# Optimization experiments

Hardware: AMD Instinct MI355X
Metric: run time of the kernel (lower is better)

## Reference

```python
import jax, jax.numpy as jnp
import numpy as np

B, SQ, SK, D, H, DFF, L = 8, 1024, 1024, 512, 8, 2048, 2
HD = D // H  # head dim = 64
EPS = 1e-5


def _ln(x, g, b):
    mu = jnp.mean(x, axis=-1, keepdims=True)
    var = jnp.mean((x - mu) ** 2, axis=-1, keepdims=True)
    return (x - mu) * jax.lax.rsqrt(var + EPS) * g + b


def setup_inputs() -> dict:
    key = jax.random.key(0)
    ks = jax.random.split(key, 16)
    std = 0.02
    inp = {
        'q': jax.random.normal(ks[0], (B, SQ, D), jnp.float32),
        'k': jax.random.normal(ks[1], (B, SK, D), jnp.float32),
        'v': jax.random.normal(ks[2], (B, SK, D), jnp.float32),
        # per-layer stacked params (weights stored [in, out])
        'WQ': jax.random.normal(ks[3], (L, D, D), jnp.float32) * std,
        'bQ': jnp.zeros((L, D), jnp.float32),
        'WK': jax.random.normal(ks[4], (L, D, D), jnp.float32) * std,
        'bK': jnp.zeros((L, D), jnp.float32),
        'WV': jax.random.normal(ks[5], (L, D, D), jnp.float32) * std,
        'bV': jnp.zeros((L, D), jnp.float32),
        'WO': jax.random.normal(ks[6], (L, D, D), jnp.float32) * std,
        'bO': jnp.zeros((L, D), jnp.float32),
        'Wf1': jax.random.normal(ks[7], (L, D, DFF), jnp.float32) * std,
        'bf1': jnp.zeros((L, DFF), jnp.float32),
        'Wf2': jax.random.normal(ks[8], (L, DFF, D), jnp.float32) * std,
        'bf2': jnp.zeros((L, D), jnp.float32),
        'ln1_g': jnp.ones((L, D), jnp.float32),
        'ln1_b': jnp.zeros((L, D), jnp.float32),
        'ln2_g': jnp.ones((L, D), jnp.float32),
        'ln2_b': jnp.zeros((L, D), jnp.float32),
        'scale': jnp.full((L,), HD ** -0.5, jnp.float32),       # self.scale init
        'extra_scale': jnp.ones((L,), jnp.float32),             # self.extra_scale init
        'gate_attn': jnp.ones((L,), jnp.float32),
        'gate_ffn': jnp.ones((L,), jnp.float32),
    }
    return inp


def reference(q, k, v, WQ, bQ, WK, bK, WV, bV, WO, bO, Wf1, bf1, Wf2, bf2,
              ln1_g, ln1_b, ln2_g, ln2_b, scale, extra_scale, gate_attn, gate_ffn):
    prev = None  # Realformer residual attention scores
    for i in range(L):
        # QKV projections -> [B, H, S, HD]
        qh = (jnp.einsum('bsd,de->bse', q, WQ[i]) + bQ[i]).reshape(B, SQ, H, HD).transpose(0, 2, 1, 3)
        kh = (jnp.einsum('bsd,de->bse', k, WK[i]) + bK[i]).reshape(B, SK, H, HD).transpose(0, 2, 1, 3)
        vh = (jnp.einsum('bsd,de->bse', v, WV[i]) + bV[i]).reshape(B, SK, H, HD).transpose(0, 2, 1, 3)
        eff_scale = scale[i] * jnp.clip(extra_scale[i], 0.01, 50.0)
        scores = jnp.einsum('bhqd,bhkd->bhqk', qh, kh) * eff_scale  # [B,H,SQ,SK]
        if prev is not None:
            scores = scores + prev
        attn = jax.nn.softmax(scores, axis=-1)
        out = jnp.einsum('bhqk,bhkd->bhqd', attn, vh)
        out = out.transpose(0, 2, 1, 3).reshape(B, SQ, D)
        out = jnp.einsum('bsd,de->bse', out, WO[i]) + bO[i]
        # gated residual + post-norm
        q = q + jax.nn.softplus(gate_attn[i]) * out
        q = _ln(q, ln1_g[i], ln1_b[i])
        # FFN (exact gelu like torch default)
        ff = jax.nn.gelu(jnp.einsum('bsd,df->bsf', q, Wf1[i]) + bf1[i], approximate=False)
        ff = jnp.einsum('bsf,fd->bsd', ff, Wf2[i]) + bf2[i]
        q = q + jax.nn.softplus(gate_ffn[i]) * ff
        q = _ln(q, ln2_g[i], ln2_b[i])
        prev = scores
    return q
```

## Files before the change

kernel.cpp:

```cpp
#include <hip/hip_runtime.h>

#define B_   8
#define SQ_  1024
#define SK_  1024
#define D_   512
#define H_   8
#define DFF_ 2048
#define L_   2
#define HD_  64
#define M_   8192

typedef __bf16 bf16;
using bf16x8 = __attribute__((ext_vector_type(8))) __bf16;
using f32x4  = __attribute__((ext_vector_type(4))) float;

__device__ inline f32x4 mfma16(bf16x8 a, bf16x8 b, f32x4 c) {
  return __builtin_amdgcn_mfma_f32_16x16x32_bf16(a, b, c, 0, 0, 0);
}

__device__ __forceinline__ void gl2lds16(const bf16* g, bf16* l) {
  __builtin_amdgcn_global_load_lds(
      (const __attribute__((address_space(1))) void*)g,
      (__attribute__((address_space(3))) void*)l, 16, 0, 0);
}

__device__ __forceinline__ float gelu_fast(float x) {
  float u = 1.5957691216f * (x + 0.044715f * x * x * x);
  return x / (1.0f + __expf(-u));
}

struct TP4 { const float* in[4]; bf16* out[4]; };
__global__ __launch_bounds__(256) void transpose4_k(TP4 p) {
  __shared__ bf16 tile[32][33];
  int z = blockIdx.z, wsel = z >> 1, l = z & 1;
  const float* inp  = p.in[wsel]  + (size_t)l * D_ * D_;
  bf16*        outp = p.out[wsel] + (size_t)l * D_ * D_;
  int c0 = blockIdx.x * 32, r0 = blockIdx.y * 32;
  int tx = threadIdx.x & 31, ty = threadIdx.x >> 5;
#pragma unroll
  for (int i = 0; i < 32; i += 8)
    tile[ty + i][tx] = (bf16)inp[(size_t)(r0 + ty + i) * D_ + c0 + tx];
  __syncthreads();
#pragma unroll
  for (int i = 0; i < 32; i += 8)
    outp[(size_t)(c0 + ty + i) * D_ + r0 + tx] = tile[tx][ty + i];
}

__global__ __launch_bounds__(256) void transpose_k(
    const float* __restrict__ in, bf16* __restrict__ out, int R, int C) {
  __shared__ bf16 tile[32][33];
  const float* inp  = in  + (size_t)blockIdx.z * R * C;
  bf16*        outp = out + (size_t)blockIdx.z * R * C;
  int c0 = blockIdx.x * 32, r0 = blockIdx.y * 32;
  int tx = threadIdx.x & 31, ty = threadIdx.x >> 5;
#pragma unroll
  for (int i = 0; i < 32; i += 8)
    tile[ty + i][tx] = (bf16)inp[(size_t)(r0 + ty + i) * C + c0 + tx];
  __syncthreads();
#pragma unroll
  for (int i = 0; i < 32; i += 8)
    outp[(size_t)(c0 + ty + i) * R + r0 + tx] = tile[tx][ty + i];
}

__global__ __launch_bounds__(256) void f2b3_k(
    const float* __restrict__ a, const float* __restrict__ b,
    const float* __restrict__ c, bf16* __restrict__ oa,
    bf16* __restrict__ ob, bf16* __restrict__ oc) {
  int which = blockIdx.y;
  const float* in = (which == 0) ? a : (which == 1) ? b : c;
  bf16* out = (which == 0) ? oa : (which == 1) ? ob : oc;
  int i = (blockIdx.x * 256 + threadIdx.x) * 4;
  float4 v = *(const float4*)&in[i];
  out[i] = (bf16)v.x; out[i + 1] = (bf16)v.y;
  out[i + 2] = (bf16)v.z; out[i + 3] = (bf16)v.w;
}

struct G256 { const bf16* A; const bf16* Bt; const float* bias; bf16* C; };

#define MFB(mh) \
  _Pragma("unroll") \
  for (int mi = 0; mi < 4; mi++) { \
    _Pragma("unroll") \
    for (int ni = 0; ni < 4; ni++) \
      acc[(mh) * 4 + mi][ni] = mfma16(a[mi], b[ni], acc[(mh) * 4 + mi][ni]); \
  }

#define PHASE(s, mh, STAGE, VM) \
  { \
    if ((mh) == 0) { \
      a[0] = ldA(s, 0); a[1] = ldA(s, 1); a[2] = ldA(s, 2); a[3] = ldA(s, 3); \
      b[0] = ldB(s, 0); b[1] = ldB(s, 1); b[2] = ldB(s, 2); b[3] = ldB(s, 3); \
    } else { \
      a[0] = ldA(s, 4); a[1] = ldA(s, 5); a[2] = ldA(s, 6); a[3] = ldA(s, 7); \
    } \
    STAGE; \
    VM; \
    __builtin_amdgcn_s_barrier(); \
    asm volatile("s_waitcnt lgkmcnt(0)" ::: "memory"); \
    __builtin_amdgcn_sched_barrier(0); \
    __builtin_amdgcn_s_setprio(1); \
    MFB(mh); \
    __builtin_amdgcn_s_setprio(0); \
    __builtin_amdgcn_s_barrier(); \
  }

__global__ __launch_bounds__(512, 2) void gemm256_k(G256 g0, G256 g1,
                                                    int Nsz, int Ksz,
                                                    int gelu) {
  __shared__ bf16 As[4 * 8192];
  __shared__ bf16 Bs[4 * 8192];
  const G256 g = blockIdx.z ? g1 : g0;
  const int tid = threadIdx.x;
  const int w = tid >> 6, lane = tid & 63;
  const int quad = lane >> 4, l16 = lane & 15;
  const int wm = w >> 2, wn = w & 3;
  const int m0 = blockIdx.x * 256, n0 = blockIdx.y * 256;
  const int NCH = Ksz >> 5;
  const int ITERS = NCH >> 2;

  const int srow = tid >> 2;
  const int ssw = ((tid & 3) ^ (srow & 3) ^ ((srow >> 2) & 3)) << 3;
  const int swr = ((quad ^ (l16 & 3) ^ (l16 >> 2)) << 3);

  auto stageA = [&](int kc, int s) {
    const bf16* gp = g.A + (size_t)(m0 + srow) * Ksz + kc * 32 + ssw;
    gl2lds16(gp, &As[s * 8192 + w * 512]);
    gl2lds16(gp + (size_t)128 * Ksz, &As[s * 8192 + 4096 + w * 512]);
  };
  auto stageB = [&](int kc, int s) {
    const bf16* gp = g.Bt + (size_t)(n0 + srow) * Ksz + kc * 32 + ssw;
    gl2lds16(gp, &Bs[s * 8192 + w * 512]);
    gl2lds16(gp + (size_t)128 * Ksz, &Bs[s * 8192 + 4096 + w * 512]);
  };
  auto ldA = [&](int s, int mi) {
    return *(const bf16x8*)&As[s * 8192 + (wm * 128 + mi * 16 + l16) * 32 + swr];
  };
  auto ldB = [&](int s, int ni) {
    return *(const bf16x8*)&Bs[s * 8192 + (wn * 64 + ni * 16 + l16) * 32 + swr];
  };

  f32x4 acc[8][4] = {};

  stageA(0, 0); stageB(0, 0);
  stageA(1, 1); stageB(1, 1);
  stageA(2, 2); stageB(2, 2);
  asm volatile("s_waitcnt vmcnt(4)" ::: "memory");
  __builtin_amdgcn_s_barrier();

  for (int it = 0; it < ITERS; ++it) {
    const int c = it * 4;
    const bool last = (it + 1 == ITERS);
    bf16x8 a[4], b[4];
    PHASE(0, 0, stageA(c + 3, 3), )
    PHASE(0, 1, stageB(c + 3, 3), )
    PHASE(1, 0, if (!last) stageA(c + 4, 0), )
    PHASE(1, 1, if (!last) stageB(c + 4, 0),
          if (!last) { asm volatile("s_waitcnt vmcnt(4)" ::: "memory"); }
          else { asm volatile("s_waitcnt vmcnt(0)" ::: "memory"); })
    PHASE(2, 0, if (!last) stageA(c + 5, 1), )
    PHASE(2, 1, if (!last) stageB(c + 5, 1), )
    PHASE(3, 0, if (!last) stageA(c + 6, 2), )
    PHASE(3, 1, if (!last) stageB(c + 6, 2),
          asm volatile("s_waitcnt vmcnt(4)" ::: "memory"))
  }

#pragma unroll
  for (int mi = 0; mi < 8; mi++)
#pragma unroll
    for (int ni = 0; ni < 4; ni++) {
      const int col = n0 + wn * 64 + ni * 16 + l16;
      const float bv = g.bias[col];
#pragma unroll
      for (int r = 0; r < 4; r++) {
        const int row = m0 + wm * 128 + mi * 16 + quad * 4 + r;
        float x = acc[mi][ni][r] + bv;
        if (gelu) x = gelu_fast(x);
        g.C[(size_t)row * Nsz + col] = (bf16)x;
      }
    }
}

__global__ __launch_bounds__(512, 2) void gemm256s_k(
    const bf16* __restrict__ A, const bf16* __restrict__ Bt,
    bf16* __restrict__ P, int Nsz, int Kstride, int Kpart) {
  __shared__ bf16 As[4 * 8192];
  __shared__ bf16 Bs[4 * 8192];
  const int z = blockIdx.z;
  const int koff = z * Kpart;
  const int tid = threadIdx.x;
  const int w = tid >> 6, lane = tid & 63;
  const int quad = lane >> 4, l16 = lane & 15;
  const int wm = w >> 2, wn = w & 3;
  const int m0 = blockIdx.x * 256, n0 = blockIdx.y * 256;
  const int ITERS = (Kpart >> 5) >> 2;

  const int srow = tid >> 2;
  const int ssw = ((tid & 3) ^ (srow & 3) ^ ((srow >> 2) & 3)) << 3;
  const int swr = ((quad ^ (l16 & 3) ^ (l16 >> 2)) << 3);

  auto stageA = [&](int kc, int s) {
    const bf16* gp = A + (size_t)(m0 + srow) * Kstride + koff + kc * 32 + ssw;
    gl2lds16(gp, &As[s * 8192 + w * 512]);
    gl2lds16(gp + (size_t)128 * Kstride, &As[s * 8192 + 4096 + w * 512]);
  };
  auto stageB = [&](int kc, int s) {
    const bf16* gp = Bt + (size_t)(n0 + srow) * Kstride + koff + kc * 32 + ssw;
    gl2lds16(gp, &Bs[s * 8192 + w * 512]);
    gl2lds16(gp + (size_t)128 * Kstride, &Bs[s * 8192 + 4096 + w * 512]);
  };
  auto ldA = [&](int s, int mi) {
    return *(const bf16x8*)&As[s * 8192 + (wm * 128 + mi * 16 + l16) * 32 + swr];
  };
  auto ldB = [&](int s, int ni) {
    return *(const bf16x8*)&Bs[s * 8192 + (wn * 64 + ni * 16 + l16) * 32 + swr];
  };

  f32x4 acc[8][4] = {};

  stageA(0, 0); stageB(0, 0);
  stageA(1, 1); stageB(1, 1);
  stageA(2, 2); stageB(2, 2);
  asm volatile("s_waitcnt vmcnt(4)" ::: "memory");
  __builtin_amdgcn_s_barrier();

  for (int it = 0; it < ITERS; ++it) {
    const int c = it * 4;
    const bool last = (it + 1 == ITERS);
    bf16x8 a[4], b[4];
    PHASE(0, 0, stageA(c + 3, 3), )
    PHASE(0, 1, stageB(c + 3, 3), )
    PHASE(1, 0, if (!last) stageA(c + 4, 0), )
    PHASE(1, 1, if (!last) stageB(c + 4, 0),
          if (!last) { asm volatile("s_waitcnt vmcnt(4)" ::: "memory"); }
          else { asm volatile("s_waitcnt vmcnt(0)" ::: "memory"); })
    PHASE(2, 0, if (!last) stageA(c + 5, 1), )
    PHASE(2, 1, if (!last) stageB(c + 5, 1), )
    PHASE(3, 0, if (!last) stageA(c + 6, 2), )
    PHASE(3, 1, if (!last) stageB(c + 6, 2),
          asm volatile("s_waitcnt vmcnt(4)" ::: "memory"))
  }

  const size_t Msz = (size_t)gridDim.x * 256;
  bf16* Pz = P + (size_t)z * Msz * Nsz;
#pragma unroll
  for (int mi = 0; mi < 8; mi++)
#pragma unroll
    for (int ni = 0; ni < 4; ni++) {
      const int col = n0 + wn * 64 + ni * 16 + l16;
#pragma unroll
      for (int r = 0; r < 4; r++) {
        const int row = m0 + wm * 128 + mi * 16 + quad * 4 + r;
        Pz[(size_t)row * Nsz + col] = (bf16)acc[mi][ni][r];
      }
    }
}

__global__ __launch_bounds__(512, 2) void gemm128_k(
    const bf16* __restrict__ A, const bf16* __restrict__ Bt,
    const float* __restrict__ bias, bf16* __restrict__ Cb,
    float* __restrict__ Cf, int Nsz, int Ksz) {
  __shared__ bf16 As[4 * 4096];
  __shared__ bf16 Bs[4 * 4096];
  const int tid = threadIdx.x;
  const int w = tid >> 6, lane = tid & 63;
  const int quad = lane >> 4, l16 = lane & 15;
  const int wm = w >> 2, wn = w & 3;
  const int m0 = blockIdx.x * 128, n0 = blockIdx.y * 128;
  const int NCH = Ksz >> 5;

  const int srow = tid >> 2;
  const int ssw = ((tid & 3) ^ (srow & 3) ^ ((srow >> 2) & 3)) << 3;
  const int swr = ((quad ^ (l16 & 3) ^ (l16 >> 2)) << 3);

  auto stageChunk = [&](int kc) {
    const int s = kc & 3;
    gl2lds16(A + (size_t)(m0 + srow) * Ksz + kc * 32 + ssw,
             &As[s * 4096 + w * 512]);
    gl2lds16(Bt + (size_t)(n0 + srow) * Ksz + kc * 32 + ssw,
             &Bs[s * 4096 + w * 512]);
  };
  auto ldA = [&](int s, int mi) {
    return *(const bf16x8*)&As[s * 4096 + (wm * 64 + mi * 16 + l16) * 32 + swr];
  };
  auto ldB = [&](int s, int ni) {
    return *(const bf16x8*)&Bs[s * 4096 + (wn * 32 + ni * 16 + l16) * 32 + swr];
  };

  f32x4 acc[4][2] = {};

  stageChunk(0); stageChunk(1); stageChunk(2);
  asm volatile("s_waitcnt vmcnt(4)" ::: "memory");
  __builtin_amdgcn_s_barrier();

  auto phase = [&](int c, int vml) {
    const int s = c & 3;
    if (vml == 4) stageChunk(c + 3);
    bf16x8 a0 = ldA(s, 0), a1 = ldA(s, 1), a2 = ldA(s, 2), a3 = ldA(s, 3);
    bf16x8 b0 = ldB(s, 0), b1 = ldB(s, 1);
    if (vml == 4)      asm volatile("s_waitcnt vmcnt(4)" ::: "memory");
    else if (vml == 2) asm volatile("s_waitcnt vmcnt(2)" ::: "memory");
    else if (vml == 0) asm volatile("s_waitcnt vmcnt(0)" ::: "memory");
    __builtin_amdgcn_s_barrier();
    asm volatile("s_waitcnt lgkmcnt(0)" ::: "memory");
    __builtin_amdgcn_sched_barrier(0);
    __builtin_amdgcn_s_setprio(1);
    acc[0][0] = mfma16(a0, b0, acc[0][0]);
    acc[0][1] = mfma16(a0, b1, acc[0][1]);
    acc[1][0] = mfma16(a1, b0, acc[1][0]);
    acc[1][1] = mfma16(a1, b1, acc[1][1]);
    acc[2][0] = mfma16(a2, b0, acc[2][0]);
    acc[2][1] = mfma16(a2, b1, acc[2][1]);
    acc[3][0] = mfma16(a3, b0, acc[3][0]);
    acc[3][1] = mfma16(a3, b1, acc[3][1]);
    __builtin_amdgcn_s_setprio(0);
    __builtin_amdgcn_s_barrier();
  };

  for (int c = 0; c + 4 <= NCH; ++c) phase(c, 4);
  phase(NCH - 3, 2);
  phase(NCH - 2, 0);
  phase(NCH - 1, -1);

#pragma unroll
  for (int mi = 0; mi < 4; mi++)
#pragma unroll
    for (int ni = 0; ni < 2; ni++) {
      const int col = n0 + wn * 32 + ni * 16 + l16;
      const float bv = bias[col];
#pragma unroll
      for (int r = 0; r < 4; r++) {
        const int row = m0 + wm * 64 + mi * 16 + quad * 4 + r;
        float x = acc[mi][ni][r] + bv;
        size_t idx = (size_t)row * Nsz + col;
        if (Cb) Cb[idx] = (bf16)x;
        if (Cf) Cf[idx] = x;
      }
    }
}

__global__ __launch_bounds__(256) void vtrans2_k(const bf16* __restrict__ vhh,
                                                 bf16* __restrict__ vt0,
                                                 bf16* __restrict__ vt1) {
  __shared__ bf16 sm[64][72];
  int kt = blockIdx.x, bh = blockIdx.y, z = blockIdx.z;
  int coloff = z ? D_ : 0;
  bf16* vt = z ? vt1 : vt0;
  int b = bh >> 3, h = bh & 7;
  int tid = threadIdx.x;
  for (int c = tid; c < 512; c += 256) {
    int key = c >> 3, off = (c & 7) * 8;
    *(uint4*)&sm[key][off] = *(const uint4*)
        &vhh[(size_t)(b * SK_ + kt * 64 + key) * (2 * D_) + coloff + h * 64 + off];
  }
  __syncthreads();
  for (int c = tid; c < 512; c += 256) {
    int hd = c >> 3, koff = (c & 7) * 8;
    bf16 tmp[8];
#pragma unroll
    for (int j = 0; j < 8; j++) tmp[j] = sm[koff + j][hd];
    *(uint4*)&vt[(size_t)(bh * 64 + hd) * SK_ + kt * 64 + koff] = *(uint4*)tmp;
  }
}

template<bool HAS0>
__global__ __launch_bounds__(256) void attn_t(
    const bf16* __restrict__ qh, const bf16* __restrict__ qh0,
    const bf16* __restrict__ kh, const bf16* __restrict__ kh0, int kstride,
    const bf16* __restrict__ vt, const float* __restrict__ scale,
    const float* __restrict__ extra, int li, bf16* __restrict__ ctx) {
  __shared__ bf16 Ks[2 * 2048];
  __shared__ bf16 K0s[HAS0 ? 2 * 2048 : 64];
  __shared__ bf16 Vs[2 * 2048];
  __shared__ bf16 Ps[4][16 * 40];
  int qt = blockIdx.x, bh = blockIdx.y;
  int b = bh >> 3, h = bh & 7;
  int tid = threadIdx.x, w = tid >> 6, lane = tid & 63;
  int quad = lane >> 4, l16 = lane & 15;
  const int rr = lane >> 2, c8 = (lane & 3) * 8;
  float eff1 = scale[li] * fminf(fmaxf(extra[li], 0.01f), 50.0f);
  float eff0 = HAS0 ? scale[li - 1] * fminf(fmaxf(extra[li - 1], 0.01f), 50.0f) : 0.f;

  bf16x8 aq[2], aq0[2];
  {
    int qrow = b * SQ_ + qt * 64 + w * 16 + l16;
    const bf16* qp = qh + (size_t)qrow * D_ + h * 64 + quad * 8;
    aq[0] = *(const bf16x8*)qp; aq[1] = *(const bf16x8*)(qp + 32);
#pragma unroll
    for (int k2 = 0; k2 < 2; k2++)
#pragma unroll
      for (int j = 0; j < 8; j++)
        aq[k2][j] = (bf16)((float)aq[k2][j] * eff1);
    if constexpr (HAS0) {
      const bf16* qp0 = qh0 + (size_t)qrow * D_ + h * 64 + quad * 8;
      aq0[0] = *(const bf16x8*)qp0; aq0[1] = *(const bf16x8*)(qp0 + 32);
#pragma unroll
      for (int k2 = 0; k2 < 2; k2++)
#pragma unroll
        for (int j = 0; j < 8; j++)
          aq0[k2][j] = (bf16)((float)aq0[k2][j] * eff0);
    }
  }
  bf16x8 ones;
#pragma unroll
  for (int j = 0; j < 8; j++) ones[j] = (bf16)1.0f;

  f32x4 o[4] = {};
  f32x4 ol = {};

  auto stage = [&](int kt, int bufi) {
#pragma unroll
    for (int ui = 0; ui < (HAS0 ? 3 : 2); ui++) {
      int u = w + ui * 4;
      if (u < 4) {
        int hf = u >> 1, g = u & 1;
        gl2lds16(&kh[(size_t)(b * SK_ + kt * 32 + g * 16 + rr) * kstride +
                     h * 64 + hf * 32 + c8],
                 &Ks[bufi * 2048 + hf * 1024 + g * 512]);
      } else if (HAS0 && u < 8) {
        int uu = u - 4; int hf = uu >> 1, g = uu & 1;
        gl2lds16(&kh0[(size_t)(b * SK_ + kt * 32 + g * 16 + rr) * kstride +
                      h * 64 + hf * 32 + c8],
                 &K0s[bufi * 2048 + hf * 1024 + g * 512]);
      } else {
        int g2 = u & 3;
        gl2lds16(&vt[(size_t)(bh * 64 + g2 * 16 + rr) * SK_ + kt * 32 + c8],
                 &Vs[bufi * 2048 + g2 * 512]);
      }
    }
  };

  stage(0, 0);
  __syncthreads();
  int buf = 0;
  for (int kt = 0; kt < SK_ / 32; kt++, buf ^= 1) {
    if (kt + 1 < SK_ / 32) stage(kt + 1, buf ^ 1);
#pragma unroll
    for (int ni = 0; ni < 2; ni++) {
      int ro = (ni * 16 + l16) * 32 + quad * 8;
      f32x4 t = {};
      t = mfma16(aq[0], *(const bf16x8*)&Ks[buf * 2048 + ro], t);
      t = mfma16(aq[1], *(const bf16x8*)&Ks[buf * 2048 + 1024 + ro], t);
      if constexpr (HAS0) {
        t = mfma16(aq0[0], *(const bf16x8*)&K0s[buf * 2048 + ro], t);
        t = mfma16(aq0[1], *(const bf16x8*)&K0s[buf * 2048 + 1024 + ro], t);
      }
#pragma unroll
      for (int r = 0; r < 4; r++)
        Ps[w][(quad * 4 + r) * 40 + ni * 16 + l16] = (bf16)__expf(t[r]);
    }
    {
      bf16x8 ap = *(const bf16x8*)&Ps[w][l16 * 40 + quad * 8];
      ol = mfma16(ap, ones, ol);
#pragma unroll
      for (int ni = 0; ni < 4; ni++)
        o[ni] = mfma16(ap,
                       *(const bf16x8*)&Vs[buf * 2048 + (ni * 16 + l16) * 32 +
                                           quad * 8],
                       o[ni]);
    }
    __syncthreads();
  }
#pragma unroll
  for (int ni = 0; ni < 4; ni++)
#pragma unroll
    for (int r = 0; r < 4; r++) {
      int row = b * SQ_ + qt * 64 + w * 16 + quad * 4 + r;
      ctx[(size_t)row * D_ + h * 64 + ni * 16 + l16] =
          (bf16)(o[ni][r] / ol[r]);
    }
}

__global__ __launch_bounds__(256) void ln_k(
    const float* __restrict__ cur_in, const float* __restrict__ add,
    const float* __restrict__ gate, const float* __restrict__ g,
    const float* __restrict__ bb, float* __restrict__ outf,
    bf16* __restrict__ outb) {
  int row = blockIdx.x, tid = threadIdx.x;
  float gv = gate[0];
  float sp = gv > 20.f ? gv : log1pf(expf(gv));
  size_t base = (size_t)row * D_;
  int c0 = tid * 2;
  float2 c2 = *(const float2*)&cur_in[base + c0];
  float2 a2 = *(const float2*)&add[base + c0];
  float x0 = c2.x + sp * a2.x, x1 = c2.y + sp * a2.y;
  float s = x0 + x1, s2 = x0 * x0 + x1 * x1;
#pragma unroll
  for (int m = 1; m < 64; m <<= 1) {
    s += __shfl_xor(s, m);
    s2 += __shfl_xor(s2, m);
  }
  __shared__ float sa[4], sb[4];
  int w = tid >> 6;
  if ((tid & 63) == 0) { sa[w] = s; sb[w] = s2; }
  __syncthreads();
  s = sa[0] + sa[1] + sa[2] + sa[3];
  s2 = sb[0] + sb[1] + sb[2] + sb[3];
  float mu = s * (1.f / D_);
  float var = s2 * (1.f / D_) - mu * mu;
  float rs = rsqrtf(var + 1e-5f);
  float y0 = (x0 - mu) * rs * g[c0] + bb[c0];
  float y1 = (x1 - mu) * rs * g[c0 + 1] + bb[c0 + 1];
  if (outf) { float2 y; y.x = y0; y.y = y1; *(float2*)&outf[base + c0] = y; }
  if (outb) { outb[base + c0] = (bf16)y0; outb[base + c0 + 1] = (bf16)y1; }
}

__global__ __launch_bounds__(256) void ln4_k(
    const float* __restrict__ cur_in, const bf16* __restrict__ P,
    const float* __restrict__ bias2, const float* __restrict__ gate,
    const float* __restrict__ g, const float* __restrict__ bb,
    float* __restrict__ outf, bf16* __restrict__ outb) {
  int row = blockIdx.x, tid = threadIdx.x;
  float gv = gate[0];
  float sp = gv > 20.f ? gv : log1pf(expf(gv));
  size_t base = (size_t)row * D_;
  int c0 = tid * 2;
  float2 c2 = *(const float2*)&cur_in[base + c0];
  float a0 = bias2[c0], a1 = bias2[c0 + 1];
  const size_t MD = (size_t)M_ * D_;
#pragma unroll
  for (int z = 0; z < 4; z++) {
    const bf16* pp = P + z * MD + base + c0;
    a0 += (float)pp[0];
    a1 += (float)pp[1];
  }
  float x0 = c2.x + sp * a0, x1 = c2.y + sp * a1;
  float s = x0 + x1, s2 = x0 * x0 + x1 * x1;
#pragma unroll
  for (int m = 1; m < 64; m <<= 1) {
    s += __shfl_xor(s, m);
    s2 += __shfl_xor(s2, m);
  }
  __shared__ float sa[4], sb[4];
  int w = tid >> 6;
  if ((tid & 63) == 0) { sa[w] = s; sb[w] = s2; }
  __syncthreads();
  s = sa[0] + sa[1] + sa[2] + sa[3];
  s2 = sb[0] + sb[1] + sb[2] + sb[3];
  float mu = s * (1.f / D_);
  float var = s2 * (1.f / D_) - mu * mu;
  float rs = rsqrtf(var + 1e-5f);
  float y0 = (x0 - mu) * rs * g[c0] + bb[c0];
  float y1 = (x1 - mu) * rs * g[c0 + 1] + bb[c0 + 1];
  if (outf) { float2 y; y.x = y0; y.y = y1; *(float2*)&outf[base + c0] = y; }
  if (outb) { outb[base + c0] = (bf16)y0; outb[base + c0 + 1] = (bf16)y1; }
}

extern "C" void kernel_launch(void* const* d_in, const int* in_sizes, int n_in,
                              void* d_out, int out_size, void* d_ws,
                              size_t ws_size, hipStream_t stream) {
  const float* qin = (const float*)d_in[0];
  const float* kin = (const float*)d_in[1];
  const float* vin = (const float*)d_in[2];
  const float* WQ  = (const float*)d_in[3];
  const float* bQ  = (const float*)d_in[4];
  const float* WK  = (const float*)d_in[5];
  const float* bK  = (const float*)d_in[6];
  const float* WV  = (const float*)d_in[7];
  const float* bV  = (const float*)d_in[8];
  const float* WO  = (const float*)d_in[9];
  const float* bO  = (const float*)d_in[10];
  const float* Wf1 = (const float*)d_in[11];
  const float* bf1 = (const float*)d_in[12];
  const float* Wf2 = (const float*)d_in[13];
  const float* bf2 = (const float*)d_in[14];
  const float* l1g = (const float*)d_in[15];
  const float* l1b = (const float*)d_in[16];
  const float* l2g = (const float*)d_in[17];
  const float* l2b = (const float*)d_in[18];
  const float* sc  = (const float*)d_in[19];
  const float* ex  = (const float*)d_in[20];
  const float* ga  = (const float*)d_in[21];
  const float* gf  = (const float*)d_in[22];

  char* p = (char*)d_ws;
  auto alloc = [&](size_t bytes) {
    void* r = (void*)p;
    p += (bytes + 255) & ~(size_t)255;
    return r;
  };
  bf16* WQt  = (bf16*)alloc((size_t)L_ * D_ * D_ * 2);
  bf16* WKt  = (bf16*)alloc((size_t)L_ * D_ * D_ * 2);
  bf16* WVt  = (bf16*)alloc((size_t)L_ * D_ * D_ * 2);
  bf16* WOt  = (bf16*)alloc((size_t)L_ * D_ * D_ * 2);
  bf16* Wf1t = (bf16*)alloc((size_t)L_ * D_ * DFF_ * 2);
  bf16* Wf2t = (bf16*)alloc((size_t)L_ * D_ * DFF_ * 2);
  float* cur  = (float*)alloc((size_t)M_ * D_ * 4);
  bf16* curb  = (bf16*)alloc((size_t)M_ * D_ * 2);
  bf16* qb    = (bf16*)alloc((size_t)M_ * D_ * 2);
  bf16* kb    = (bf16*)alloc((size_t)M_ * D_ * 2);
  bf16* vb    = (bf16*)alloc((size_t)M_ * D_ * 2);
  bf16* khh   = (bf16*)alloc((size_t)M_ * 2 * D_ * 2);
  bf16* vhh   = (bf16*)alloc((size_t)M_ * 2 * D_ * 2);
  bf16* qh0b  = (bf16*)alloc((size_t)M_ * D_ * 2);
  bf16* qh1b  = (bf16*)alloc((size_t)M_ * D_ * 2);
  bf16* vt0   = (bf16*)alloc((size_t)M_ * D_ * 2);
  bf16* vt1   = (bf16*)alloc((size_t)M_ * D_ * 2);
  bf16* ctx   = (bf16*)alloc((size_t)M_ * D_ * 2);
  float* proj  = (float*)alloc((size_t)M_ * D_ * 4);
  float* ffout = (float*)alloc((size_t)M_ * D_ * 4);
  bf16* parts  = (bf16*)proj;
  bf16* ffmid  = (bf16*)alloc((size_t)M_ * DFF_ * 2);
  (void)ffout;

  TP4 tp; tp.in[0] = WQ; tp.in[1] = WK; tp.in[2] = WV; tp.in[3] = WO;
  tp.out[0] = WQt; tp.out[1] = WKt; tp.out[2] = WVt; tp.out[3] = WOt;
  transpose4_k<<<dim3(16, 16, 8), 256, 0, stream>>>(tp);
  transpose_k<<<dim3(DFF_ / 32, D_ / 32, L_), 256, 0, stream>>>(Wf1, Wf1t, D_, DFF_);
  transpose_k<<<dim3(D_ / 32, DFF_ / 32, L_), 256, 0, stream>>>(Wf2, Wf2t, DFF_, D_);
  f2b3_k<<<dim3((M_ * D_) / 1024, 3), 256, 0, stream>>>(qin, kin, vin, qb, kb, vb);

  G256 gk; gk.A = kb; gk.Bt = WKt; gk.bias = bK; gk.C = khh;
  G256 gvv; gvv.A = vb; gvv.Bt = WVt; gvv.bias = bV; gvv.C = vhh;
  gemm256_k<<<dim3(M_ / 256, (2 * D_) / 256, 2), 512, 0, stream>>>(
      gk, gvv, 2 * D_, D_, 0);
  vtrans2_k<<<dim3(SK_ / 64, B_ * H_, 2), 256, 0, stream>>>(vhh, vt0, vt1);
  gemm128_k<<<dim3(M_ / 128, 4), 512, 0, stream>>>(
      qb, WQt, bQ, qh0b, nullptr, D_, D_);

  for (int li = 0; li < L_; li++) {
    if (li > 0)
      gemm128_k<<<dim3(M_ / 128, 4), 512, 0, stream>>>(
          curb, WQt + (size_t)li * D_ * D_, bQ + li * D_, qh1b, nullptr, D_, D_);
    if (li == 0)
      attn_t<false><<<dim3(SQ_ / 64, B_ * H_), 256, 0, stream>>>(
          qh0b, qh0b, khh, khh, 2 * D_, vt0, sc, ex, 0, ctx);
    else
      attn_t<true><<<dim3(SQ_ / 64, B_ * H_), 256, 0, stream>>>(
          qh1b, qh0b, khh + (size_t)li * D_, khh, 2 * D_, vt1, sc, ex, 1, ctx);
    gemm128_k<<<dim3(M_ / 128, 4), 512, 0, stream>>>(
        ctx, WOt + (size_t)li * D_ * D_, bO + li * D_, nullptr, proj, D_, D_);
    ln_k<<<M_, 256, 0, stream>>>((li == 0) ? qin : cur, proj, ga + li,
                                 l1g + li * D_, l1b + li * D_, cur, curb);
    G256 gf1; gf1.A = curb; gf1.Bt = Wf1t + (size_t)li * D_ * DFF_;
    gf1.bias = bf1 + li * DFF_; gf1.C = ffmid;
    gemm256_k<<<dim3(M_ / 256, DFF_ / 256, 1), 512, 0, stream>>>(
        gf1, gf1, DFF_, D_, 1);
    gemm256s_k<<<dim3(M_ / 256, D_ / 256, 4), 512, 0, stream>>>(
        ffmid, Wf2t + (size_t)li * DFF_ * D_, parts, D_, DFF_, DFF_ / 4);
    ln4_k<<<M_, 256, 0, stream>>>(cur, parts, bf2 + li * D_, gf + li,
                                  l2g + li * D_, l2b + li * D_,
                                  (li == L_ - 1) ? (float*)d_out : cur,
                                  (li == L_ - 1) ? nullptr : curb);
  }
}
```

Baseline: 498.1 us.

## Load K/V fragments directly from global in attention, dropping LDS staging

The attention kernel stops double-buffering K, K0 and V tiles into shared memory with global_load_lds and block barriers. Each wave now loads its MFMA operand fragments straight from global memory into registers every iteration. This removes the LDS traffic and the per-iteration __syncthreads. In exchange, the four waves of a block each re-read the same K/V data through cache, and there is no explicit prefetch, so load latency may be exposed.

```diff
diff --git a/kernel.cpp b/kernel.cpp
--- a/kernel.cpp
+++ b/kernel.cpp
@@ -368,15 +368,11 @@
     const bf16* __restrict__ kh, const bf16* __restrict__ kh0, int kstride,
     const bf16* __restrict__ vt, const float* __restrict__ scale,
     const float* __restrict__ extra, int li, bf16* __restrict__ ctx) {
-  __shared__ bf16 Ks[2 * 2048];
-  __shared__ bf16 K0s[HAS0 ? 2 * 2048 : 64];
-  __shared__ bf16 Vs[2 * 2048];
   __shared__ bf16 Ps[4][16 * 40];
   int qt = blockIdx.x, bh = blockIdx.y;
   int b = bh >> 3, h = bh & 7;
   int tid = threadIdx.x, w = tid >> 6, lane = tid & 63;
   int quad = lane >> 4, l16 = lane & 15;
-  const int rr = lane >> 2, c8 = (lane & 3) * 8;
   float eff1 = scale[li] * fminf(fmaxf(extra[li], 0.01f), 50.0f);
   float eff0 = HAS0 ? scale[li - 1] * fminf(fmaxf(extra[li - 1], 0.01f), 50.0f) : 0.f;
 
@@ -407,58 +403,45 @@
   f32x4 o[4] = {};
   f32x4 ol = {};
 
-  auto stage = [&](int kt, int bufi) {
-#pragma unroll
-    for (int ui = 0; ui < (HAS0 ? 3 : 2); ui++) {
-      int u = w + ui * 4;
-      if (u < 4) {
-        int hf = u >> 1, g = u & 1;
-        gl2lds16(&kh[(size_t)(b * SK_ + kt * 32 + g * 16 + rr) * kstride +
-                     h * 64 + hf * 32 + c8],
-                 &Ks[bufi * 2048 + hf * 1024 + g * 512]);
-      } else if (HAS0 && u < 8) {
-        int uu = u - 4; int hf = uu >> 1, g = uu & 1;
-        gl2lds16(&kh0[(size_t)(b * SK_ + kt * 32 + g * 16 + rr) * kstride +
-                      h * 64 + hf * 32 + c8],
-                 &K0s[bufi * 2048 + hf * 1024 + g * 512]);
-      } else {
-        int g2 = u & 3;
-        gl2lds16(&vt[(size_t)(bh * 64 + g2 * 16 + rr) * SK_ + kt * 32 + c8],
-                 &Vs[bufi * 2048 + g2 * 512]);
+  const bf16* kbase  = kh + (size_t)(b * SK_ + l16) * kstride + h * 64 + quad * 8;
+  const bf16* k0base = kh0 + (size_t)(b * SK_ + l16) * kstride + h * 64 + quad * 8;
+  const bf16* vbase  = vt + (size_t)(bh * 64 + l16) * SK_ + quad * 8;
+
+  for (int kt = 0; kt < SK_ / 32; kt++) {
+    bf16x8 bk[2][2], bk0[2][2], bv[4];
+#pragma unroll
+    for (int ni = 0; ni < 2; ni++) {
+      const bf16* kp = kbase + (size_t)(kt * 32 + ni * 16) * kstride;
+      bk[ni][0] = *(const bf16x8*)kp;
+      bk[ni][1] = *(const bf16x8*)(kp + 32);
+      if constexpr (HAS0) {
+        const bf16* kp0 = k0base + (size_t)(kt * 32 + ni * 16) * kstride;
+        bk0[ni][0] = *(const bf16x8*)kp0;
+        bk0[ni][1] = *(const bf16x8*)(kp0 + 32);
       }
     }
-  };
-
-  stage(0, 0);
-  __syncthreads();
-  int buf = 0;
-  for (int kt = 0; kt < SK_ / 32; kt++, buf ^= 1) {
-    if (kt + 1 < SK_ / 32) stage(kt + 1, buf ^ 1);
+#pragma unroll
+    for (int ni = 0; ni < 4; ni++)
+      bv[ni] = *(const bf16x8*)(vbase + (size_t)(ni * 16) * SK_ + kt * 32);
+
 #pragma unroll
     for (int ni = 0; ni < 2; ni++) {
-      int ro = (ni * 16 + l16) * 32 + quad * 8;
       f32x4 t = {};
-      t = mfma16(aq[0], *(const bf16x8*)&Ks[buf * 2048 + ro], t);
-      t = mfma16(aq[1], *(const bf16x8*)&Ks[buf * 2048 + 1024 + ro], t);
+      t = mfma16(aq[0], bk[ni][0], t);
+      t = mfma16(aq[1], bk[ni][1], t);
       if constexpr (HAS0) {
-        t = mfma16(aq0[0], *(const bf16x8*)&K0s[buf * 2048 + ro], t);
-        t = mfma16(aq0[1], *(const bf16x8*)&K0s[buf * 2048 + 1024 + ro], t);
+        t = mfma16(aq0[0], bk0[ni][0], t);
+        t = mfma16(aq0[1], bk0[ni][1], t);
       }
 #pragma unroll
       for (int r = 0; r < 4; r++)
         Ps[w][(quad * 4 + r) * 40 + ni * 16 + l16] = (bf16)__expf(t[r]);
     }
-    {
-      bf16x8 ap = *(const bf16x8*)&Ps[w][l16 * 40 + quad * 8];
-      ol = mfma16(ap, ones, ol);
-#pragma unroll
-      for (int ni = 0; ni < 4; ni++)
-        o[ni] = mfma16(ap,
-                       *(const bf16x8*)&Vs[buf * 2048 + (ni * 16 + l16) * 32 +
-                                           quad * 8],
-                       o[ni]);
-    }
-    __syncthreads();
+    bf16x8 ap = *(const bf16x8*)&Ps[w][l16 * 40 + quad * 8];
+    ol = mfma16(ap, ones, ol);
+#pragma unroll
+    for (int ni = 0; ni < 4; ni++)
+      o[ni] = mfma16(ap, bv[ni], o[ni]);
   }
 #pragma unroll
   for (int ni = 0; ni < 4; ni++)
```

New measurement: 696.3 us. 1.4x slower.

## Software-pipeline attention loop so PV MFMAs of previous tile overlap QK of current

Applied to the files above, without the earlier changes.

The attention inner loop is restructured into a two-stage software pipeline. The P and V fragments of tile kt are held in registers, and their PV MFMAs run during iteration kt+1, interleaved with the QK MFMAs and exp of the next tile. The aim is to hide the LDS round-trip latency of writing and reading back P, and the exp latency, behind independent matrix work. In exchange it holds more live registers (two sets of P and V fragments), which could lower occupancy.

```diff
diff --git a/kernel.cpp b/kernel.cpp
--- a/kernel.cpp
+++ b/kernel.cpp
@@ -431,35 +431,56 @@
 
   stage(0, 0);
   __syncthreads();
-  int buf = 0;
-  for (int kt = 0; kt < SK_ / 32; kt++, buf ^= 1) {
-    if (kt + 1 < SK_ / 32) stage(kt + 1, buf ^ 1);
-#pragma unroll
-    for (int ni = 0; ni < 2; ni++) {
-      int ro = (ni * 16 + l16) * 32 + quad * 8;
-      f32x4 t = {};
-      t = mfma16(aq[0], *(const bf16x8*)&Ks[buf * 2048 + ro], t);
-      t = mfma16(aq[1], *(const bf16x8*)&Ks[buf * 2048 + 1024 + ro], t);
+
+  auto body = [&](int kt, int bufi, bf16x8& ap_c, bf16x8 (&bv_c)[4],
+                  bf16x8& ap_p, bf16x8 (&bv_p)[4], bool dopv) {
+    if (kt + 1 < SK_ / 32) stage(kt + 1, bufi ^ 1);
+#pragma unroll
+    for (int ni = 0; ni < 4; ni++)
+      bv_c[ni] = *(const bf16x8*)&Vs[bufi * 2048 + (ni * 16 + l16) * 32 +
+                                     quad * 8];
+    f32x4 t0 = {}, t1 = {};
+    {
+      int ro0 = l16 * 32 + quad * 8;
+      int ro1 = (16 + l16) * 32 + quad * 8;
+      t0 = mfma16(aq[0], *(const bf16x8*)&Ks[bufi * 2048 + ro0], t0);
+      t0 = mfma16(aq[1], *(const bf16x8*)&Ks[bufi * 2048 + 1024 + ro0], t0);
+      t1 = mfma16(aq[0], *(const bf16x8*)&Ks[bufi * 2048 + ro1], t1);
+      t1 = mfma16(aq[1], *(const bf16x8*)&Ks[bufi * 2048 + 1024 + ro1], t1);
       if constexpr (HAS0) {
-        t = mfma16(aq0[0], *(const bf16x8*)&K0s[buf * 2048 + ro], t);
-        t = mfma16(aq0[1], *(const bf16x8*)&K0s[buf * 2048 + 1024 + ro], t);
+        t0 = mfma16(aq0[0], *(const bf16x8*)&K0s[bufi * 2048 + ro0], t0);
+        t0 = mfma16(aq0[1], *(const bf16x8*)&K0s[bufi * 2048 + 1024 + ro0], t0);
+        t1 = mfma16(aq0[0], *(const bf16x8*)&K0s[bufi * 2048 + ro1], t1);
+        t1 = mfma16(aq0[1], *(const bf16x8*)&K0s[bufi * 2048 + 1024 + ro1], t1);
       }
-#pragma unroll
-      for (int r = 0; r < 4; r++)
-        Ps[w][(quad * 4 + r) * 40 + ni * 16 + l16] = (bf16)__expf(t[r]);
-    }
-    {
-      bf16x8 ap = *(const bf16x8*)&Ps[w][l16 * 40 + quad * 8];
-      ol = mfma16(ap, ones, ol);
+    }
+    if (dopv) {
+      ol = mfma16(ap_p, ones, ol);
 #pragma unroll
       for (int ni = 0; ni < 4; ni++)
-        o[ni] = mfma16(ap,
-                       *(const bf16x8*)&Vs[buf * 2048 + (ni * 16 + l16) * 32 +
-                                           quad * 8],
-                       o[ni]);
-    }
+        o[ni] = mfma16(ap_p, bv_p[ni], o[ni]);
+    }
+#pragma unroll
+    for (int r = 0; r < 4; r++) {
+      Ps[w][(quad * 4 + r) * 40 + l16]      = (bf16)__expf(t0[r]);
+      Ps[w][(quad * 4 + r) * 40 + 16 + l16] = (bf16)__expf(t1[r]);
+    }
+    ap_c = *(const bf16x8*)&Ps[w][l16 * 40 + quad * 8];
     __syncthreads();
-  }
+  };
+
+  bf16x8 apA, apB, bvA[4], bvB[4];
+  body(0, 0, apA, bvA, apB, bvB, false);
+  for (int kt = 1; kt < 31; kt += 2) {
+    body(kt, 1, apB, bvB, apA, bvA, true);
+    body(kt + 1, 0, apA, bvA, apB, bvB, true);
+  }
+  body(31, 1, apB, bvB, apA, bvA, true);
+  ol = mfma16(apB, ones, ol);
+#pragma unroll
+  for (int ni = 0; ni < 4; ni++)
+    o[ni] = mfma16(apB, bvB[ni], o[ni]);
+
 #pragma unroll
   for (int ni = 0; ni < 4; ni++)
 #pragma unroll
```

New measurement: 510.6 us. 2.5% more time.
